# Performance work log

Hardware: AMD Instinct MI355X
Metric: run time of the kernel (lower is better)

The kernel has to match this reference:

```python
import jax, jax.numpy as jnp
import numpy as np

GI_DIM = 1220
HID = 150
GIJ = 3 * GI_DIM + 60  # 3720


def setup_inputs() -> dict:
    key = jax.random.key(0)
    ks = jax.random.split(key, 16)
    N, P = 50000, 100000
    inp = {
        "g_i": jax.random.normal(ks[0], (N, GI_DIM), jnp.float32),
        "mention_scores": jax.random.normal(ks[1], (N,), jnp.float32),
        "dist_emb": jax.random.normal(ks[2], (9, 20), jnp.float32) * 0.1,
        "genre_emb": jax.random.normal(ks[3], (8, 20), jnp.float32) * 0.1,
        "speaker_emb": jax.random.normal(ks[4], (3, 20), jnp.float32) * 0.1,
        "W1": jax.random.normal(ks[5], (GIJ, HID), jnp.float32) / np.sqrt(GIJ),
        "b1": jnp.zeros((HID,), jnp.float32),
        "W2": jax.random.normal(ks[6], (HID, HID), jnp.float32) / np.sqrt(HID),
        "b2": jnp.zeros((HID,), jnp.float32),
        "W3": jax.random.normal(ks[7], (HID, 1), jnp.float32) / np.sqrt(HID),
        "b3": jnp.zeros((1,), jnp.float32),
        "mention_ids": jax.random.randint(ks[8], (P,), 0, N, jnp.int64 if jax.config.jax_enable_x64 else jnp.int32),
        "antecedent_ids": jax.random.randint(ks[9], (P,), 0, N, jnp.int32),
        "distance_ids": jax.random.randint(ks[10], (P,), 0, 9, jnp.int32),
        "genre_ids": jax.random.randint(ks[11], (P,), 0, 8, jnp.int32),
        "speaker_ids": jax.random.randint(ks[12], (P,), 0, 3, jnp.int32),
    }
    return inp


def reference(g_i, mention_scores, dist_emb, genre_emb, speaker_emb,
              W1, b1, W2, b2, W3, b3,
              mention_ids, antecedent_ids, distance_ids, genre_ids, speaker_ids):
    # phi: [P, 60] pair features (distance, genre, speaker embeddings)
    phi = jnp.concatenate([dist_emb[distance_ids],
                           genre_emb[genre_ids],
                           speaker_emb[speaker_ids]], axis=1)
    i_g = g_i[mention_ids]      # [P, GI_DIM]
    j_g = g_i[antecedent_ids]   # [P, GI_DIM]
    pairs = jnp.concatenate([i_g, j_g, i_g * j_g, phi], axis=1)  # [P, GIJ]
    h = jax.nn.relu(pairs @ W1 + b1)
    h = jax.nn.relu(h @ W2 + b2)
    pairwise = (h @ W3 + b3)[:, 0]  # [P]
    sij = mention_scores[mention_ids] + mention_scores[antecedent_ids] + pairwise
    return sij
```

## Files before the change

### kernel.cpp

```cpp
#include <hip/hip_runtime.h>

#define GI  1220
#define KP  1280
#define BK  128
#define NCH (KP / BK)
#define NP  192
#define ABW 320

typedef __bf16        bf16x8 __attribute__((ext_vector_type(8)));
typedef float         f32x4  __attribute__((ext_vector_type(4)));
typedef unsigned int  u32x4  __attribute__((ext_vector_type(4)));
typedef unsigned int  u32x2  __attribute__((ext_vector_type(2)));

__device__ __forceinline__ unsigned short f2bf(float f) {
  __bf16 h = (__bf16)f;
  return __builtin_bit_cast(unsigned short, h);
}
__device__ __forceinline__ float bf2f(unsigned short u) {
  return (float)__builtin_bit_cast(__bf16, u);
}
__device__ __forceinline__ unsigned int pk2(float a, float b) {
  return (unsigned int)f2bf(a) | ((unsigned int)f2bf(b) << 16);
}

__global__ void prep_kernel(const float* __restrict__ W1, const float* __restrict__ W2,
                            const float* __restrict__ b1,
                            const float* __restrict__ de, const float* __restrict__ ge,
                            const float* __restrict__ se,
                            unsigned short* __restrict__ W1ab_t,
                            unsigned short* __restrict__ W1c_t,
                            unsigned short* __restrict__ W2_t,
                            float* __restrict__ projs) {
  int idx = blockIdx.x * 256 + threadIdx.x;
  const int R1 = ABW * KP, R2 = NP * KP, R3 = NP * NP, R4 = 20 * NP;
  if (idx < R1) {
    int n = idx / KP, k = idx % KP;
    float v = 0.f;
    if (k < GI) {
      if (n < 150)                 v = W1[k * 150 + n];
      else if (n >= 160 && n < 310) v = W1[(GI + k) * 150 + (n - 160)];
    }
    W1ab_t[idx] = f2bf(v);
    return;
  }
  idx -= R1;
  if (idx < R2) {
    int n = idx / KP, k = idx % KP;
    float v = (k < GI && n < 150) ? W1[(2 * GI + k) * 150 + n] : 0.f;
    W1c_t[idx] = f2bf(v);
    return;
  }
  idx -= R2;
  if (idx < R3) {
    int n = idx / NP, k = idx % NP;
    float v = (n < 150 && k < 150) ? W2[k * 150 + n] : 0.f;
    W2_t[idx] = f2bf(v);
    return;
  }
  idx -= R3;
  if (idx < R4) {
    int r = idx / NP, n = idx % NP;
    float v = 0.f;
    if (n < 150) {
      if (r < 9) {
        v = b1[n];
        for (int t = 0; t < 20; ++t) v += de[r * 20 + t] * W1[(3660 + t) * 150 + n];
      } else if (r < 17) {
        int q = r - 9;
        for (int t = 0; t < 20; ++t) v += ge[q * 20 + t] * W1[(3680 + t) * 150 + n];
      } else {
        int q = r - 17;
        for (int t = 0; t < 20; ++t) v += se[q * 20 + t] * W1[(3700 + t) * 150 + n];
      }
    }
    projs[idx] = v;
  }
}

__global__ __launch_bounds__(256, 3)
void ab_kernel(const float* __restrict__ g, const unsigned short* __restrict__ W1ab_t,
               unsigned short* __restrict__ AB, int N) {
  __shared__ __attribute__((aligned(16))) unsigned short sX[64 * 136];
  const int t = threadIdx.x;
  const int m0 = blockIdx.x * 64;
  const int w = t >> 6, lane = t & 63, quad = lane >> 4, lm = lane & 15;

  f32x4 acc[4][5];
#pragma unroll
  for (int a = 0; a < 4; ++a)
#pragma unroll
    for (int b = 0; b < 5; ++b) { acc[a][b].x = 0.f; acc[a][b].y = 0.f; acc[a][b].z = 0.f; acc[a][b].w = 0.f; }

  const int r = t >> 2, s = t & 3;
  int row = m0 + r; if (row >= N) row = N - 1;
  const float* gr = g + (long)row * GI;

  for (int c = 0; c < NCH; ++c) {
    __syncthreads();
#pragma unroll
    for (int i = 0; i < 8; ++i) {
      int k = c * BK + i * 16 + s * 4;
      u32x2 pk; pk.x = 0u; pk.y = 0u;
      if (k < GI) {
        f32x4 x = *(const f32x4*)(gr + k);
        pk.x = pk2(x.x, x.y);
        pk.y = pk2(x.z, x.w);
      }
      *(u32x2*)&sX[r * 136 + i * 16 + s * 4] = pk;
    }
    __syncthreads();
#pragma unroll
    for (int kk = 0; kk < 4; ++kk) {
      bf16x8 af[4];
#pragma unroll
      for (int mi = 0; mi < 4; ++mi)
        af[mi] = __builtin_bit_cast(bf16x8, *(const u32x4*)&sX[(mi * 16 + lm) * 136 + kk * 32 + quad * 8]);
#pragma unroll
      for (int tl = 0; tl < 5; ++tl) {
        int n = (w * 5 + tl) * 16 + lm;
        bf16x8 bfr = __builtin_bit_cast(bf16x8, *(const u32x4*)(W1ab_t + n * KP + c * BK + kk * 32 + quad * 8));
#pragma unroll
        for (int mi = 0; mi < 4; ++mi)
          acc[mi][tl] = __builtin_amdgcn_mfma_f32_16x16x32_bf16(af[mi], bfr, acc[mi][tl], 0, 0, 0);
      }
    }
  }
#pragma unroll
  for (int mi = 0; mi < 4; ++mi)
#pragma unroll
    for (int reg = 0; reg < 4; ++reg) {
      int m = m0 + mi * 16 + quad * 4 + reg;
      if (m < N) {
#pragma unroll
        for (int tl = 0; tl < 5; ++tl) {
          int n = (w * 5 + tl) * 16 + lm;
          AB[(long)m * ABW + n] = f2bf(acc[mi][tl][reg]);
        }
      }
    }
}

__global__ __launch_bounds__(256, 3)
void pair_kernel(const float* __restrict__ g, const float* __restrict__ msc,
                 const unsigned short* __restrict__ AB,
                 const unsigned short* __restrict__ W1c_t,
                 const unsigned short* __restrict__ W2_t,
                 const float* __restrict__ projs,
                 const float* __restrict__ b2, const float* __restrict__ W3,
                 const float* __restrict__ b3,
                 const int* __restrict__ mid, const int* __restrict__ aid,
                 const int* __restrict__ did, const int* __restrict__ gid,
                 const int* __restrict__ sid,
                 float* __restrict__ out, int N, int P) {
  __shared__ __attribute__((aligned(16))) unsigned short sXh1[64 * 200];
  __shared__ __attribute__((aligned(16))) unsigned short sBias[64 * NP];
  __shared__ int sM[64], sA[64], sD[64], sG[64], sS[64];
  __shared__ float sScore[64];

  const int t = threadIdx.x;
  const int p0 = blockIdx.x * 64;
  const int w = t >> 6, lane = t & 63, quad = lane >> 4, lm = lane & 15;

  if (t < 64) {
    int p = p0 + t;
    int m_ = 0, a_ = 0, d_ = 0, g_ = 0, s_ = 0;
    float sc = 0.f;
    if (p < P) {
      m_ = mid[p]; a_ = aid[p]; d_ = did[p]; g_ = gid[p]; s_ = sid[p];
      sc = msc[m_] + msc[a_];
    }
    sM[t] = m_; sA[t] = a_; sD[t] = d_; sG[t] = g_; sS[t] = s_;
    sScore[t] = sc;
  }
  __syncthreads();

  const int r = t >> 2, s = t & 3;
  const float* gm = g + (long)sM[r] * GI;
  const float* ga = g + (long)sA[r] * GI;

  {
    const unsigned short* Ar = AB + (long)sM[r] * ABW;
    const unsigned short* Br = AB + (long)sA[r] * ABW + 160;
    const float* dp = projs + sD[r] * NP;
    const float* gp = projs + (9 + sG[r]) * NP;
    const float* sp = projs + (17 + sS[r]) * NP;
#pragma unroll
    for (int j = 0; j < 6; ++j) {
      int n = s * 48 + j * 8;
      f32x4 p0v = *(const f32x4*)(dp + n) + *(const f32x4*)(gp + n) + *(const f32x4*)(sp + n);
      f32x4 p1v = *(const f32x4*)(dp + n + 4) + *(const f32x4*)(gp + n + 4) + *(const f32x4*)(sp + n + 4);
      if (n < 160) {
        u32x4 a8 = *(const u32x4*)(Ar + n);
        u32x4 b8 = *(const u32x4*)(Br + n);
        p0v.x += bf2f(a8.x & 0xffff) + bf2f(b8.x & 0xffff);
        p0v.y += bf2f(a8.x >> 16)    + bf2f(b8.x >> 16);
        p0v.z += bf2f(a8.y & 0xffff) + bf2f(b8.y & 0xffff);
        p0v.w += bf2f(a8.y >> 16)    + bf2f(b8.y >> 16);
        p1v.x += bf2f(a8.z & 0xffff) + bf2f(b8.z & 0xffff);
        p1v.y += bf2f(a8.z >> 16)    + bf2f(b8.z >> 16);
        p1v.z += bf2f(a8.w & 0xffff) + bf2f(b8.w & 0xffff);
        p1v.w += bf2f(a8.w >> 16)    + bf2f(b8.w >> 16);
      }
      u32x4 o;
      o.x = pk2(p0v.x, p0v.y); o.y = pk2(p0v.z, p0v.w);
      o.z = pk2(p1v.x, p1v.y); o.w = pk2(p1v.z, p1v.w);
      *(u32x4*)&sBias[r * NP + n] = o;
    }
  }

  f32x4 acc[4][3];
#pragma unroll
  for (int a = 0; a < 4; ++a)
#pragma unroll
    for (int b = 0; b < 3; ++b) { acc[a][b].x = 0.f; acc[a][b].y = 0.f; acc[a][b].z = 0.f; acc[a][b].w = 0.f; }

  for (int c = 0; c < NCH; ++c) {
    __syncthreads();
#pragma unroll
    for (int i = 0; i < 8; ++i) {
      int k = c * BK + i * 16 + s * 4;
      u32x2 pk; pk.x = 0u; pk.y = 0u;
      if (k < GI) {
        f32x4 x = *(const f32x4*)(gm + k);
        f32x4 y = *(const f32x4*)(ga + k);
        pk.x = pk2(x.x * y.x, x.y * y.y);
        pk.y = pk2(x.z * y.z, x.w * y.w);
      }
      *(u32x2*)&sXh1[r * 136 + i * 16 + s * 4] = pk;
    }
    __syncthreads();
#pragma unroll
    for (int kk = 0; kk < 4; ++kk) {
      bf16x8 af[4];
#pragma unroll
      for (int mi = 0; mi < 4; ++mi)
        af[mi] = __builtin_bit_cast(bf16x8, *(const u32x4*)&sXh1[(mi * 16 + lm) * 136 + kk * 32 + quad * 8]);
#pragma unroll
      for (int tl = 0; tl < 3; ++tl) {
        int n = (w * 3 + tl) * 16 + lm;
        bf16x8 bfr = __builtin_bit_cast(bf16x8, *(const u32x4*)(W1c_t + n * KP + c * BK + kk * 32 + quad * 8));
#pragma unroll
        for (int mi = 0; mi < 4; ++mi)
          acc[mi][tl] = __builtin_amdgcn_mfma_f32_16x16x32_bf16(af[mi], bfr, acc[mi][tl], 0, 0, 0);
      }
    }
  }

  __syncthreads();
#pragma unroll
  for (int mi = 0; mi < 4; ++mi)
#pragma unroll
    for (int tl = 0; tl < 3; ++tl) {
      int n = (w * 3 + tl) * 16 + lm;
#pragma unroll
      for (int reg = 0; reg < 4; ++reg) {
        int m = mi * 16 + quad * 4 + reg;
        float v = acc[mi][tl][reg] + bf2f(sBias[m * NP + n]);
        v = fmaxf(v, 0.f);
        sXh1[m * 200 + n] = f2bf(v);
      }
    }
  __syncthreads();

  f32x4 acc2[4][3];
#pragma unroll
  for (int a = 0; a < 4; ++a)
#pragma unroll
    for (int b = 0; b < 3; ++b) { acc2[a][b].x = 0.f; acc2[a][b].y = 0.f; acc2[a][b].z = 0.f; acc2[a][b].w = 0.f; }
#pragma unroll
  for (int kk = 0; kk < 6; ++kk) {
    bf16x8 af[4];
#pragma unroll
    for (int mi = 0; mi < 4; ++mi)
      af[mi] = __builtin_bit_cast(bf16x8, *(const u32x4*)&sXh1[(mi * 16 + lm) * 200 + kk * 32 + quad * 8]);
#pragma unroll
    for (int tl = 0; tl < 3; ++tl) {
      int n = (w * 3 + tl) * 16 + lm;
      bf16x8 bfr = __builtin_bit_cast(bf16x8, *(const u32x4*)(W2_t + n * NP + kk * 32 + quad * 8));
#pragma unroll
      for (int mi = 0; mi < 4; ++mi)
        acc2[mi][tl] = __builtin_amdgcn_mfma_f32_16x16x32_bf16(af[mi], bfr, acc2[mi][tl], 0, 0, 0);
    }
  }

#pragma unroll
  for (int mi = 0; mi < 4; ++mi)
#pragma unroll
    for (int tl = 0; tl < 3; ++tl) {
      int n = (w * 3 + tl) * 16 + lm;
      float bb = (n < 150) ? b2[n] : 0.f;
#pragma unroll
      for (int reg = 0; reg < 4; ++reg) {
        int m = mi * 16 + quad * 4 + reg;
        float v = acc2[mi][tl][reg] + bb;
        v = fmaxf(v, 0.f);
        sBias[m * NP + n] = f2bf(v);
      }
    }
  __syncthreads();

  {
    float sum = 0.f;
#pragma unroll
    for (int j = 0; j < 48; ++j) {
      int n = s * 48 + j;
      if (n < 150) sum += bf2f(sBias[r * NP + n]) * W3[n];
    }
    sum += __shfl_xor(sum, 1);
    sum += __shfl_xor(sum, 2);
    if (s == 0) {
      int p = p0 + r;
      if (p < P) out[p] = sScore[r] + sum + b3[0];
    }
  }
}

extern "C" void kernel_launch(void* const* d_in, const int* in_sizes, int n_in,
                              void* d_out, int out_size, void* d_ws, size_t ws_size,
                              hipStream_t stream) {
  (void)n_in; (void)out_size; (void)ws_size;
  const float* g   = (const float*)d_in[0];
  const float* msc = (const float*)d_in[1];
  const float* de  = (const float*)d_in[2];
  const float* ge  = (const float*)d_in[3];
  const float* se  = (const float*)d_in[4];
  const float* W1  = (const float*)d_in[5];
  const float* b1  = (const float*)d_in[6];
  const float* W2  = (const float*)d_in[7];
  const float* b2  = (const float*)d_in[8];
  const float* W3  = (const float*)d_in[9];
  const float* b3  = (const float*)d_in[10];
  const int* mid = (const int*)d_in[11];
  const int* aid = (const int*)d_in[12];
  const int* did = (const int*)d_in[13];
  const int* gid = (const int*)d_in[14];
  const int* sid = (const int*)d_in[15];
  const int N = in_sizes[0] / GI;
  const int P = in_sizes[11];
  float* out = (float*)d_out;

  char* ws = (char*)d_ws;
  size_t off = 0;
  auto alloc = [&](size_t bytes) { char* p = ws + off; off = (off + bytes + 255) & ~(size_t)255; return p; };
  unsigned short* AB     = (unsigned short*)alloc((size_t)N * ABW * 2);
  unsigned short* W1ab_t = (unsigned short*)alloc((size_t)ABW * KP * 2);
  unsigned short* W1c_t  = (unsigned short*)alloc((size_t)NP * KP * 2);
  unsigned short* W2_t   = (unsigned short*)alloc((size_t)NP * NP * 2);
  float* projs           = (float*)alloc((size_t)20 * NP * 4);

  const int prep_total = ABW * KP + NP * KP + NP * NP + 20 * NP;
  prep_kernel<<<(prep_total + 255) / 256, 256, 0, stream>>>(W1, W2, b1, de, ge, se,
                                                            W1ab_t, W1c_t, W2_t, projs);
  ab_kernel<<<(N + 63) / 64, 256, 0, stream>>>(g, W1ab_t, AB, N);
  pair_kernel<<<(P + 63) / 64, 256, 0, stream>>>(g, msc, AB, W1c_t, W2_t, projs,
                                                 b2, W3, b3, mid, aid, did, gid, sid,
                                                 out, N, P);
}
```

Measured before the change: 773.3 us.

## Switch to fp16 MFMA and cache fp16 copy of g_i for pair gathers

Moves all matrix operands from bf16 to fp16, using fp16 MFMA instructions. The ab_kernel now also writes a padded fp16 copy of g_i to workspace, so the pair kernel gathers half-size rows and multiplies them in packed fp16 instead of loading fp32 rows and converting. This cuts gather bandwidth in the pair kernel, the dominant cost, at the price of an extra write of N×1280 halves and fp16 range limits on activations and products.

```diff
diff --git a/kernel.cpp b/kernel.cpp
--- a/kernel.cpp
+++ b/kernel.cpp
@@ -7,20 +7,20 @@
 #define NP  192
 #define ABW 320
 
-typedef __bf16        bf16x8 __attribute__((ext_vector_type(8)));
-typedef float         f32x4  __attribute__((ext_vector_type(4)));
-typedef unsigned int  u32x4  __attribute__((ext_vector_type(4)));
-typedef unsigned int  u32x2  __attribute__((ext_vector_type(2)));
-
-__device__ __forceinline__ unsigned short f2bf(float f) {
-  __bf16 h = (__bf16)f;
-  return __builtin_bit_cast(unsigned short, h);
-}
-__device__ __forceinline__ float bf2f(unsigned short u) {
-  return (float)__builtin_bit_cast(__bf16, u);
-}
-__device__ __forceinline__ unsigned int pk2(float a, float b) {
-  return (unsigned int)f2bf(a) | ((unsigned int)f2bf(b) << 16);
+typedef _Float16      f16;
+typedef _Float16      f16x8 __attribute__((ext_vector_type(8)));
+typedef float         f32x4 __attribute__((ext_vector_type(4)));
+typedef unsigned int  u32x4 __attribute__((ext_vector_type(4)));
+typedef unsigned int  u32x2 __attribute__((ext_vector_type(2)));
+
+__device__ __forceinline__ unsigned short f2h(float f) {
+  return __builtin_bit_cast(unsigned short, (f16)f);
+}
+__device__ __forceinline__ float h2f(unsigned short u) {
+  return (float)__builtin_bit_cast(f16, u);
+}
+__device__ __forceinline__ unsigned int pkh(float a, float b) {
+  return (unsigned int)f2h(a) | ((unsigned int)f2h(b) << 16);
 }
 
 __global__ void prep_kernel(const float* __restrict__ W1, const float* __restrict__ W2,
@@ -40,21 +40,21 @@
       if (n < 150)                 v = W1[k * 150 + n];
       else if (n >= 160 && n < 310) v = W1[(GI + k) * 150 + (n - 160)];
     }
-    W1ab_t[idx] = f2bf(v);
+    W1ab_t[idx] = f2h(v);
     return;
   }
   idx -= R1;
   if (idx < R2) {
     int n = idx / KP, k = idx % KP;
     float v = (k < GI && n < 150) ? W1[(2 * GI + k) * 150 + n] : 0.f;
-    W1c_t[idx] = f2bf(v);
+    W1c_t[idx] = f2h(v);
     return;
   }
   idx -= R2;
   if (idx < R3) {
     int n = idx / NP, k = idx % NP;
     float v = (n < 150 && k < 150) ? W2[k * 150 + n] : 0.f;
-    W2_t[idx] = f2bf(v);
+    W2_t[idx] = f2h(v);
     return;
   }
   idx -= R3;
@@ -79,7 +79,7 @@
 
 __global__ __launch_bounds__(256, 3)
 void ab_kernel(const float* __restrict__ g, const unsigned short* __restrict__ W1ab_t,
-               unsigned short* __restrict__ AB, int N) {
+               unsigned short* __restrict__ AB, unsigned short* __restrict__ gb, int N) {
   __shared__ __attribute__((aligned(16))) unsigned short sX[64 * 136];
   const int t = threadIdx.x;
   const int m0 = blockIdx.x * 64;
@@ -94,34 +94,36 @@
   const int r = t >> 2, s = t & 3;
   int row = m0 + r; if (row >= N) row = N - 1;
   const float* gr = g + (long)row * GI;
+  unsigned short* gbr = gb + (long)row * KP;
 
   for (int c = 0; c < NCH; ++c) {
     __syncthreads();
 #pragma unroll
     for (int i = 0; i < 8; ++i) {
       int k = c * BK + i * 16 + s * 4;
-      u32x2 pk; pk.x = 0u; pk.y = 0u;
+      u32x2 ph; ph.x = 0u; ph.y = 0u;
       if (k < GI) {
         f32x4 x = *(const f32x4*)(gr + k);
-        pk.x = pk2(x.x, x.y);
-        pk.y = pk2(x.z, x.w);
-      }
-      *(u32x2*)&sX[r * 136 + i * 16 + s * 4] = pk;
+        ph.x = pkh(x.x, x.y);
+        ph.y = pkh(x.z, x.w);
+      }
+      *(u32x2*)&sX[r * 136 + i * 16 + s * 4] = ph;
+      *(u32x2*)(gbr + k) = ph;
     }
     __syncthreads();
 #pragma unroll
     for (int kk = 0; kk < 4; ++kk) {
-      bf16x8 af[4];
+      f16x8 af[4];
 #pragma unroll
       for (int mi = 0; mi < 4; ++mi)
-        af[mi] = __builtin_bit_cast(bf16x8, *(const u32x4*)&sX[(mi * 16 + lm) * 136 + kk * 32 + quad * 8]);
+        af[mi] = __builtin_bit_cast(f16x8, *(const u32x4*)&sX[(mi * 16 + lm) * 136 + kk * 32 + quad * 8]);
 #pragma unroll
       for (int tl = 0; tl < 5; ++tl) {
         int n = (w * 5 + tl) * 16 + lm;
-        bf16x8 bfr = __builtin_bit_cast(bf16x8, *(const u32x4*)(W1ab_t + n * KP + c * BK + kk * 32 + quad * 8));
+        f16x8 bfr = __builtin_bit_cast(f16x8, *(const u32x4*)(W1ab_t + n * KP + c * BK + kk * 32 + quad * 8));
 #pragma unroll
         for (int mi = 0; mi < 4; ++mi)
-          acc[mi][tl] = __builtin_amdgcn_mfma_f32_16x16x32_bf16(af[mi], bfr, acc[mi][tl], 0, 0, 0);
+          acc[mi][tl] = __builtin_amdgcn_mfma_f32_16x16x32_f16(af[mi], bfr, acc[mi][tl], 0, 0, 0);
       }
     }
   }
@@ -134,14 +136,14 @@
 #pragma unroll
         for (int tl = 0; tl < 5; ++tl) {
           int n = (w * 5 + tl) * 16 + lm;
-          AB[(long)m * ABW + n] = f2bf(acc[mi][tl][reg]);
+          AB[(long)m * ABW + n] = f2h(acc[mi][tl][reg]);
         }
       }
     }
 }
 
 __global__ __launch_bounds__(256, 3)
-void pair_kernel(const float* __restrict__ g, const float* __restrict__ msc,
+void pair_kernel(const unsigned short* __restrict__ gb, const float* __restrict__ msc,
                  const unsigned short* __restrict__ AB,
                  const unsigned short* __restrict__ W1c_t,
                  const unsigned short* __restrict__ W2_t,
@@ -175,8 +177,8 @@
   __syncthreads();
 
   const int r = t >> 2, s = t & 3;
-  const float* gm = g + (long)sM[r] * GI;
-  const float* ga = g + (long)sA[r] * GI;
+  const unsigned short* gbm = gb + (long)sM[r] * KP;
+  const unsigned short* gba = gb + (long)sA[r] * KP;
 
   {
     const unsigned short* Ar = AB + (long)sM[r] * ABW;
@@ -192,18 +194,18 @@
       if (n < 160) {
         u32x4 a8 = *(const u32x4*)(Ar + n);
         u32x4 b8 = *(const u32x4*)(Br + n);
-        p0v.x += bf2f(a8.x & 0xffff) + bf2f(b8.x & 0xffff);
-        p0v.y += bf2f(a8.x >> 16)    + bf2f(b8.x >> 16);
-        p0v.z += bf2f(a8.y & 0xffff) + bf2f(b8.y & 0xffff);
-        p0v.w += bf2f(a8.y >> 16)    + bf2f(b8.y >> 16);
-        p1v.x += bf2f(a8.z & 0xffff) + bf2f(b8.z & 0xffff);
-        p1v.y += bf2f(a8.z >> 16)    + bf2f(b8.z >> 16);
-        p1v.z += bf2f(a8.w & 0xffff) + bf2f(b8.w & 0xffff);
-        p1v.w += bf2f(a8.w >> 16)    + bf2f(b8.w >> 16);
+        p0v.x += h2f((unsigned short)(a8.x & 0xffff)) + h2f((unsigned short)(b8.x & 0xffff));
+        p0v.y += h2f((unsigned short)(a8.x >> 16))    + h2f((unsigned short)(b8.x >> 16));
+        p0v.z += h2f((unsigned short)(a8.y & 0xffff)) + h2f((unsigned short)(b8.y & 0xffff));
+        p0v.w += h2f((unsigned short)(a8.y >> 16))    + h2f((unsigned short)(b8.y >> 16));
+        p1v.x += h2f((unsigned short)(a8.z & 0xffff)) + h2f((unsigned short)(b8.z & 0xffff));
+        p1v.y += h2f((unsigned short)(a8.z >> 16))    + h2f((unsigned short)(b8.z >> 16));
+        p1v.z += h2f((unsigned short)(a8.w & 0xffff)) + h2f((unsigned short)(b8.w & 0xffff));
+        p1v.w += h2f((unsigned short)(a8.w >> 16))    + h2f((unsigned short)(b8.w >> 16));
       }
       u32x4 o;
-      o.x = pk2(p0v.x, p0v.y); o.y = pk2(p0v.z, p0v.w);
-      o.z = pk2(p1v.x, p1v.y); o.w = pk2(p1v.z, p1v.w);
+      o.x = pkh(p0v.x, p0v.y); o.y = pkh(p0v.z, p0v.w);
+      o.z = pkh(p1v.x, p1v.y); o.w = pkh(p1v.z, p1v.w);
       *(u32x4*)&sBias[r * NP + n] = o;
     }
   }
@@ -217,31 +219,27 @@
   for (int c = 0; c < NCH; ++c) {
     __syncthreads();
 #pragma unroll
-    for (int i = 0; i < 8; ++i) {
-      int k = c * BK + i * 16 + s * 4;
-      u32x2 pk; pk.x = 0u; pk.y = 0u;
-      if (k < GI) {
-        f32x4 x = *(const f32x4*)(gm + k);
-        f32x4 y = *(const f32x4*)(ga + k);
-        pk.x = pk2(x.x * y.x, x.y * y.y);
-        pk.y = pk2(x.z * y.z, x.w * y.w);
-      }
-      *(u32x2*)&sXh1[r * 136 + i * 16 + s * 4] = pk;
+    for (int i = 0; i < 4; ++i) {
+      int k = c * BK + i * 32 + s * 8;
+      f16x8 xm = __builtin_bit_cast(f16x8, *(const u32x4*)(gbm + k));
+      f16x8 xa = __builtin_bit_cast(f16x8, *(const u32x4*)(gba + k));
+      f16x8 pm = xm * xa;
+      *(u32x4*)&sXh1[r * 136 + i * 32 + s * 8] = __builtin_bit_cast(u32x4, pm);
     }
     __syncthreads();
 #pragma unroll
     for (int kk = 0; kk < 4; ++kk) {
-      bf16x8 af[4];
+      f16x8 af[4];
 #pragma unroll
       for (int mi = 0; mi < 4; ++mi)
-        af[mi] = __builtin_bit_cast(bf16x8, *(const u32x4*)&sXh1[(mi * 16 + lm) * 136 + kk * 32 + quad * 8]);
+        af[mi] = __builtin_bit_cast(f16x8, *(const u32x4*)&sXh1[(mi * 16 + lm) * 136 + kk * 32 + quad * 8]);
 #pragma unroll
       for (int tl = 0; tl < 3; ++tl) {
         int n = (w * 3 + tl) * 16 + lm;
-        bf16x8 bfr = __builtin_bit_cast(bf16x8, *(const u32x4*)(W1c_t + n * KP + c * BK + kk * 32 + quad * 8));
+        f16x8 bfr = __builtin_bit_cast(f16x8, *(const u32x4*)(W1c_t + n * KP + c * BK + kk * 32 + quad * 8));
 #pragma unroll
         for (int mi = 0; mi < 4; ++mi)
-          acc[mi][tl] = __builtin_amdgcn_mfma_f32_16x16x32_bf16(af[mi], bfr, acc[mi][tl], 0, 0, 0);
+          acc[mi][tl] = __builtin_amdgcn_mfma_f32_16x16x32_f16(af[mi], bfr, acc[mi][tl], 0, 0, 0);
       }
     }
   }
@@ -255,9 +253,9 @@
 #pragma unroll
       for (int reg = 0; reg < 4; ++reg) {
         int m = mi * 16 + quad * 4 + reg;
-        float v = acc[mi][tl][reg] + bf2f(sBias[m * NP + n]);
+        float v = acc[mi][tl][reg] + h2f(sBias[m * NP + n]);
         v = fmaxf(v, 0.f);
-        sXh1[m * 200 + n] = f2bf(v);
+        sXh1[m * 200 + n] = f2h(v);
       }
     }
   __syncthreads();
@@ -269,17 +267,17 @@
     for (int b = 0; b < 3; ++b) { acc2[a][b].x = 0.f; acc2[a][b].y = 0.f; acc2[a][b].z = 0.f; acc2[a][b].w = 0.f; }
 #pragma unroll
   for (int kk = 0; kk < 6; ++kk) {
-    bf16x8 af[4];
+    f16x8 af[4];
 #pragma unroll
     for (int mi = 0; mi < 4; ++mi)
-      af[mi] = __builtin_bit_cast(bf16x8, *(const u32x4*)&sXh1[(mi * 16 + lm) * 200 + kk * 32 + quad * 8]);
+      af[mi] = __builtin_bit_cast(f16x8, *(const u32x4*)&sXh1[(mi * 16 + lm) * 200 + kk * 32 + quad * 8]);
 #pragma unroll
     for (int tl = 0; tl < 3; ++tl) {
       int n = (w * 3 + tl) * 16 + lm;
-      bf16x8 bfr = __builtin_bit_cast(bf16x8, *(const u32x4*)(W2_t + n * NP + kk * 32 + quad * 8));
+      f16x8 bfr = __builtin_bit_cast(f16x8, *(const u32x4*)(W2_t + n * NP + kk * 32 + quad * 8));
 #pragma unroll
       for (int mi = 0; mi < 4; ++mi)
-        acc2[mi][tl] = __builtin_amdgcn_mfma_f32_16x16x32_bf16(af[mi], bfr, acc2[mi][tl], 0, 0, 0);
+        acc2[mi][tl] = __builtin_amdgcn_mfma_f32_16x16x32_f16(af[mi], bfr, acc2[mi][tl], 0, 0, 0);
     }
   }
 
@@ -294,7 +292,7 @@
         int m = mi * 16 + quad * 4 + reg;
         float v = acc2[mi][tl][reg] + bb;
         v = fmaxf(v, 0.f);
-        sBias[m * NP + n] = f2bf(v);
+        sBias[m * NP + n] = f2h(v);
       }
     }
   __syncthreads();
@@ -304,7 +302,7 @@
 #pragma unroll
     for (int j = 0; j < 48; ++j) {
       int n = s * 48 + j;
-      if (n < 150) sum += bf2f(sBias[r * NP + n]) * W3[n];
+      if (n < 150) sum += h2f(sBias[r * NP + n]) * W3[n];
     }
     sum += __shfl_xor(sum, 1);
     sum += __shfl_xor(sum, 2);
@@ -342,6 +340,7 @@
   char* ws = (char*)d_ws;
   size_t off = 0;
   auto alloc = [&](size_t bytes) { char* p = ws + off; off = (off + bytes + 255) & ~(size_t)255; return p; };
+  unsigned short* gb     = (unsigned short*)alloc((size_t)N * KP * 2);
   unsigned short* AB     = (unsigned short*)alloc((size_t)N * ABW * 2);
   unsigned short* W1ab_t = (unsigned short*)alloc((size_t)ABW * KP * 2);
   unsigned short* W1c_t  = (unsigned short*)alloc((size_t)NP * KP * 2);
@@ -351,8 +350,8 @@
   const int prep_total = ABW * KP + NP * KP + NP * NP + 20 * NP;
   prep_kernel<<<(prep_total + 255) / 256, 256, 0, stream>>>(W1, W2, b1, de, ge, se,
                                                             W1ab_t, W1c_t, W2_t, projs);
-  ab_kernel<<<(N + 63) / 64, 256, 0, stream>>>(g, W1ab_t, AB, N);
-  pair_kernel<<<(P + 63) / 64, 256, 0, stream>>>(g, msc, AB, W1c_t, W2_t, projs,
+  ab_kernel<<<(N + 63) / 64, 256, 0, stream>>>(g, W1ab_t, AB, gb, N);
+  pair_kernel<<<(P + 63) / 64, 256, 0, stream>>>(gb, msc, AB, W1c_t, W2_t, projs,
                                                  b2, W3, b3, mid, aid, did, gid, sid,
                                                  out, N, P);
 }
```

New measurement: 781.5 us. About the same (+1.1%).
